# Kernel optimization log

Measured on AMD Instinct MI355X. Metric: run time of the kernel, lower is better.

Reference implementation:

```python
import math
import jax, jax.numpy as jnp
import numpy as np

HEADS = 8


def setup_inputs() -> dict:
    key = jax.random.key(0)
    ks = jax.random.split(key, 8)
    B, L, S, C = 2, 1024, 2048, 1280
    CORR = 256  # native seg_corr resolution; nearest-upsampled x4 to (1024, 1024)
    sc = 0.02
    return {
        "hidden_states": jax.random.normal(ks[0], (B, L, C), jnp.float32),
        "encoder_hidden_states": jax.random.normal(ks[1], (B, S, C), jnp.float32),
        "seg_corr": jax.random.randint(ks[2], (B, CORR, CORR), 0, 2, jnp.int32),
        "Wq": jax.random.normal(ks[3], (C, C), jnp.float32) * sc,
        "Wk": jax.random.normal(ks[4], (C, C), jnp.float32) * sc,
        "Wv": jax.random.normal(ks[5], (C, C), jnp.float32) * sc,
        "Wo": jax.random.normal(ks[6], (C, C), jnp.float32) * sc,
        "bo": jnp.zeros((C,), jnp.float32),
    }


def reference(hidden_states, encoder_hidden_states, seg_corr, Wq, Wk, Wv, Wo, bo):
    B, L, C = hidden_states.shape
    S = encoder_hidden_states.shape[1]
    H = HEADS
    d = C // H

    # projections -> [B, H, L, d] / [B, H, S, d]
    q = (hidden_states @ Wq).reshape(B, L, H, d).transpose(0, 2, 1, 3)
    k = (encoder_hidden_states @ Wk).reshape(B, S, H, d).transpose(0, 2, 1, 3)
    v = (encoder_hidden_states @ Wv).reshape(B, S, H, d).transpose(0, 2, 1, 3)

    scale = 1.0 / math.sqrt(d)
    scores = jnp.einsum("bhld,bhsd->bhls", q, k) * scale  # [B, H, L, S]

    half = S // 2  # S == 2L in the match-attention branch
    # nearest-neighbor upsample of seg_corr to (L, half) == integer repeat
    rL = L // seg_corr.shape[1]
    rS = half // seg_corr.shape[2]
    corr = jnp.repeat(jnp.repeat(seg_corr, rL, axis=1), rS, axis=2)[:, None]  # [B,1,L,half]

    # hard correlation mask on the second half of keys (reference-image tokens)
    masked = jnp.where(corr == 1, scores[..., half:], jnp.float32(-jnp.inf))
    scores = jnp.concatenate([scores[..., :half], masked], axis=-1)

    attn_weight = jax.nn.softmax(scores, axis=-1)  # dropout_p = 0.0
    out = jnp.einsum("bhls,bhsd->bhld", attn_weight, v)
    out = out.transpose(0, 2, 1, 3).reshape(B, L, C)

    out = out @ Wo + bo            # to_out[0]; to_out[1] dropout is identity at p=0
    out = out + hidden_states      # residual connection; rescale_output_factor = 1
    return out
```

## Files before the change

### kernel.cpp

```cpp
#include <hip/hip_runtime.h>

typedef unsigned short u16;
typedef unsigned int   u32;
typedef unsigned char  u8;

using bf16x8 = __attribute__((ext_vector_type(8))) __bf16;
using f32x4  = __attribute__((ext_vector_type(4))) float;

__device__ __forceinline__ u16 f2bf(float f) {
    u32 u = __float_as_uint(f);
    return (u16)((u + 0x7FFFu + ((u >> 16) & 1u)) >> 16);
}

#define MFMA(a, b, c) __builtin_amdgcn_mfma_f32_16x16x32_bf16((a), (b), (c), 0, 0, 0)
#define EXP2(x) __builtin_amdgcn_exp2f(x)

__device__ __forceinline__ void gll16(const u16* g, u16* l) {
    __builtin_amdgcn_global_load_lds(
        (const __attribute__((address_space(1))) void*)g,
        (__attribute__((address_space(3))) void*)l, 16, 0, 0);
}

__global__ __launch_bounds__(256) void wtrans_kernel(
    const float* __restrict__ W0, const float* __restrict__ W1,
    const float* __restrict__ W2, const float* __restrict__ W3,
    u16* __restrict__ T0, u16* __restrict__ T1,
    u16* __restrict__ T2, u16* __restrict__ T3) {
    const int N = 1280;
    const int z = blockIdx.z;
    const float* W = (z == 0) ? W0 : (z == 1) ? W1 : (z == 2) ? W2 : W3;
    u16* T = (z == 0) ? T0 : (z == 1) ? T1 : (z == 2) ? T2 : T3;
    __shared__ float t[32][33];
    const int bx = blockIdx.x * 32, by = blockIdx.y * 32;
    const int x = threadIdx.x, ty = threadIdx.y;
#pragma unroll
    for (int j = 0; j < 4; j++) {
        const int y = ty + j * 8;
        t[y][x] = W[(size_t)(by + y) * N + (bx + x)];
    }
    __syncthreads();
#pragma unroll
    for (int j = 0; j < 4; j++) {
        const int y = ty + j * 8;
        T[(size_t)(bx + y) * N + (by + x)] = f2bf(t[x][y]);
    }
}

__global__ __launch_bounds__(256) void conv2_kernel(const float* __restrict__ in0,
                                                    u16* __restrict__ out0,
                                                    const float* __restrict__ in1,
                                                    u16* __restrict__ out1) {
    const int bid = blockIdx.x;
    const float* in = (bid < 1280) ? in0 : in1;
    u16* out = (bid < 1280) ? out0 : out1;
    const int i = ((bid < 1280) ? bid : bid - 1280) * 256 + threadIdx.x;
    const float4 a = ((const float4*)in)[i * 2];
    const float4 b = ((const float4*)in)[i * 2 + 1];
    union { uint4 u; u16 s[8]; } cv;
    cv.s[0] = f2bf(a.x); cv.s[1] = f2bf(a.y); cv.s[2] = f2bf(a.z); cv.s[3] = f2bf(a.w);
    cv.s[4] = f2bf(b.x); cv.s[5] = f2bf(b.y); cv.s[6] = f2bf(b.z); cv.s[7] = f2bf(b.w);
    ((uint4*)out)[i] = cv.u;
}

template <int MI, bool TRANSC, bool EPI>
__global__ __launch_bounds__(256) void gemm2_kernel(
    const u16* __restrict__ A, const u16* __restrict__ Bt, void* __restrict__ Cp,
    const float* __restrict__ bias, const float* __restrict__ resid,
    const int M, const int N, const int K) {
    __shared__ __align__(16) u16 Al[2][MI * 32 * 64];
    __shared__ __align__(16) u16 Bl[2][128 * 64];
    const int tid = threadIdx.x;
    const int lane = tid & 63, w = tid >> 6;
    const int wr = w >> 1, wc = w & 1;
    const int lr = lane & 15, lq = lane >> 4;
    const int m0 = blockIdx.y * (MI * 32), n0 = blockIdx.x * 128;

    const int f_r = tid >> 3;
    const int srcch = (tid & 7) ^ ((tid >> 3) & 7);
    const int ldst = (tid & 192) * 8;

    const f32x4 fzero = {0.f, 0.f, 0.f, 0.f};
    f32x4 acc[MI][4];
#pragma unroll
    for (int i = 0; i < MI; i++)
#pragma unroll
        for (int j = 0; j < 4; j++) acc[i][j] = fzero;

    const int nkt = K >> 6;

#define STAGE(buf, kt)                                                          \
    {                                                                           \
        const int k0s = (kt) << 6;                                              \
        _Pragma("unroll")                                                       \
        for (int i = 0; i < MI; i++) {                                          \
            const int r = i * 32 + f_r;                                         \
            gll16(&A[(size_t)(m0 + r) * K + k0s + srcch * 8],                   \
                  &Al[buf][i * 2048 + ldst]);                                   \
        }                                                                       \
        _Pragma("unroll")                                                       \
        for (int i = 0; i < 4; i++) {                                           \
            const int r = i * 32 + f_r;                                         \
            gll16(&Bt[(size_t)(n0 + r) * K + k0s + srcch * 8],                  \
                  &Bl[buf][i * 2048 + ldst]);                                   \
        }                                                                       \
    }

    STAGE(0, 0);
    asm volatile("s_waitcnt vmcnt(0)" ::: "memory");
    __syncthreads();
    int cur = 0;
    for (int kt = 0; kt < nkt; kt++) {
        if (kt + 1 < nkt) STAGE(cur ^ 1, kt + 1);
#pragma unroll
        for (int ks = 0; ks < 2; ks++) {
            bf16x8 af[MI], bfv[4];
#pragma unroll
            for (int mi = 0; mi < MI; mi++) {
                const int rowA = wr * (MI * 16) + mi * 16 + lr;
                af[mi] = *(const bf16x8*)&Al[cur][rowA * 64 +
                                                  (((ks * 4 + lq) ^ (rowA & 7)) << 3)];
            }
#pragma unroll
            for (int ni = 0; ni < 4; ni++) {
                const int rowB = wc * 64 + ni * 16 + lr;
                bfv[ni] = *(const bf16x8*)&Bl[cur][rowB * 64 +
                                                   (((ks * 4 + lq) ^ (rowB & 7)) << 3)];
            }
#pragma unroll
            for (int mi = 0; mi < MI; mi++)
#pragma unroll
                for (int ni = 0; ni < 4; ni++)
                    acc[mi][ni] = MFMA(af[mi], bfv[ni], acc[mi][ni]);
        }
        asm volatile("s_waitcnt vmcnt(0)" ::: "memory");
        __syncthreads();
        cur ^= 1;
    }
#undef STAGE

#pragma unroll
    for (int mi = 0; mi < MI; mi++)
#pragma unroll
        for (int ni = 0; ni < 4; ni++)
#pragma unroll
            for (int j = 0; j < 4; j++) {
                const int row = m0 + wr * (MI * 16) + mi * 16 + lq * 4 + j;
                const int col = n0 + wc * 64 + ni * 16 + lr;
                const float v = acc[mi][ni][j];
                if (EPI) {
                    ((float*)Cp)[(size_t)row * N + col] =
                        v + bias[col] + resid[(size_t)row * N + col];
                } else if (TRANSC) {
                    ((u16*)Cp)[((size_t)(col >> 11) * 1280 + row) * 2048 +
                               (col & 2047)] = f2bf(v);
                } else {
                    ((u16*)Cp)[(size_t)row * N + col] = f2bf(v);
                }
            }
}

__global__ __launch_bounds__(256) void attn_kernel(
    const u16* __restrict__ qb, const u16* __restrict__ kb,
    const u16* __restrict__ vtb, const int* __restrict__ seg,
    u16* __restrict__ ao) {
    __shared__ __align__(16) u16 arena[14080];
    const int KL = 0;
    const int VT = 5376;
    const int PT = 11776;
    const int SG = 13056;
    u8* segl8 = (u8*)&arena[SG];

    const int tid = threadIdx.x;
    const int lane = tid & 63, w = tid >> 6;
    const int qg = w >> 1, kc = w & 1;
    const int lr = lane & 15, lq = lane >> 4;
    const int id = blockIdx.x;
    const int h = id & 7, bz = (id >> 3) & 1, qt = id >> 4;

#pragma unroll
    for (int i = 0; i < 2; i++) {
        const int4 v =
            *(const int4*)&seg[(size_t)(bz * 256 + qt * 8) * 256 + tid * 8 + i * 4];
        segl8[tid * 8 + i * 4 + 0] = (u8)v.x;
        segl8[tid * 8 + i * 4 + 1] = (u8)v.y;
        segl8[tid * 8 + i * 4 + 2] = (u8)v.z;
        segl8[tid * 8 + i * 4 + 3] = (u8)v.w;
    }

    bf16x8 qf[5];
    {
        const size_t qrow =
            (size_t)(bz * 1024 + qt * 32 + qg * 16 + lr) * 1280 + h * 160;
#pragma unroll
        for (int ks = 0; ks < 5; ks++)
            qf[ks] = *(const bf16x8*)&qb[qrow + ks * 32 + lq * 8];
    }

    const int nk0 = tid, nk1 = tid + 256;
    const int nv0 = tid, nv1 = tid + 256;
    const bool exK = (tid < 128);
    const int ne = exK ? (512 + tid) : (384 + tid);
    const int gok0 = (nk0 / 20) * 1280 + (nk0 % 20) * 8;
    const int lok0 = (nk0 / 20) * 168 + (nk0 % 20) * 8;
    const int gok1 = (nk1 / 20) * 1280 + (nk1 % 20) * 8;
    const int lok1 = (nk1 / 20) * 168 + (nk1 % 20) * 8;
    const int gov0 = (nv0 >> 2) * 2048 + (nv0 & 3) * 8;
    const int lov0 = (nv0 >> 2) * 40 + (nv0 & 3) * 8;
    const int gov1 = (nv1 >> 2) * 2048 + (nv1 & 3) * 8;
    const int lov1 = (nv1 >> 2) * 40 + (nv1 & 3) * 8;
    const int goe = exK ? ((ne / 20) * 1280 + (ne % 20) * 8)
                        : ((ne >> 2) * 2048 + (ne & 3) * 8);
    const int loe = exK ? ((ne / 20) * 168 + (ne % 20) * 8)
                        : ((ne >> 2) * 40 + (ne & 3) * 8);

    const u16* kP = kb + (size_t)(bz * 2048) * 1280 + h * 160;
    const u16* vP = vtb + (size_t)(bz * 1280 + h * 160) * 2048;

    const f32x4 fzero = {0.f, 0.f, 0.f, 0.f};
    f32x4 oacc[5];
#pragma unroll
    for (int d = 0; d < 5; d++) oacc[d] = fzero;
    f32x4 oaccL = fzero;
    const float sc2 = 0.11405508f;
    bf16x8 ones8;
#pragma unroll
    for (int e = 0; e < 8; e++) {
        const u16 one = 0x3F80;
        ones8[e] = *(const __bf16*)&one;
    }
    u16* ptq = &arena[PT + qg * 640];

    uint4 rk0 = *(const uint4*)&kP[gok0];
    uint4 rk1 = *(const uint4*)&kP[gok1];
    uint4 rv0 = *(const uint4*)&vP[gov0];
    uint4 rv1 = *(const uint4*)&vP[gov1];
    uint4 re  = exK ? *(const uint4*)&kP[goe] : *(const uint4*)&vP[goe];

    for (int kt = 0; kt < 64; kt++) {
        __syncthreads();
        *(uint4*)&arena[KL + lok0] = rk0;
        *(uint4*)&arena[KL + lok1] = rk1;
        *(uint4*)&arena[VT + lov0] = rv0;
        *(uint4*)&arena[VT + lov1] = rv1;
        if (exK) *(uint4*)&arena[KL + loe] = re;
        else     *(uint4*)&arena[VT + loe] = re;
        kP += 40960;
        vP += 32;
        __syncthreads();

        if (kt + 1 < 64) {
            rk0 = *(const uint4*)&kP[gok0];
            rk1 = *(const uint4*)&kP[gok1];
            rv0 = *(const uint4*)&vP[gov0];
            rv1 = *(const uint4*)&vP[gov1];
            re  = exK ? *(const uint4*)&kP[goe] : *(const uint4*)&vP[goe];
        }

        const u16* kbase = &arena[KL + (kc * 16 + lr) * 168 + lq * 8];
        f32x4 sA = fzero, sB = fzero;
        sA = MFMA(qf[0], *(const bf16x8*)&kbase[0],   sA);
        sB = MFMA(qf[1], *(const bf16x8*)&kbase[32],  sB);
        sA = MFMA(qf[2], *(const bf16x8*)&kbase[64],  sA);
        sB = MFMA(qf[3], *(const bf16x8*)&kbase[96],  sB);
        sA = MFMA(qf[4], *(const bf16x8*)&kbase[128], sA);

        float msk = 0.f;
        if (kt >= 32) {
            const int sg = (kt - 32) * 8 + kc * 4 + (lr >> 2);
            msk = segl8[(qg * 4 + lq) * 256 + sg] ? 0.f : -1e30f;
        }
#pragma unroll
        for (int j = 0; j < 4; j++) {
            const float e = EXP2(fmaf(sA[j] + sB[j], sc2, msk));
            *(__bf16*)&ptq[(lq * 4 + j) * 40 + kc * 16 + lr] = (__bf16)e;
        }
        __syncthreads();

        const bf16x8 pa = *(const bf16x8*)&ptq[lr * 40 + lq * 8];
        oaccL = MFMA(pa, ones8, oaccL);
#pragma unroll
        for (int nt2 = 0; nt2 < 5; nt2++) {
            const bf16x8 bv = *(const bf16x8*)
                &arena[VT + (kc * 80 + nt2 * 16 + lr) * 40 + lq * 8];
            oacc[nt2] = MFMA(pa, bv, oacc[nt2]);
        }
    }

    float inv[4];
#pragma unroll
    for (int j = 0; j < 4; j++) inv[j] = 1.f / oaccL[j];
#pragma unroll
    for (int nt2 = 0; nt2 < 5; nt2++)
#pragma unroll
        for (int j = 0; j < 4; j++) {
            const int row = qt * 32 + qg * 16 + lq * 4 + j;
            const int col = h * 160 + kc * 80 + nt2 * 16 + lr;
            *(__bf16*)&ao[(size_t)(bz * 1024 + row) * 1280 + col] =
                (__bf16)(oacc[nt2][j] * inv[j]);
        }
}

extern "C" void kernel_launch(void* const* d_in, const int* in_sizes, int n_in,
                              void* d_out, int out_size, void* d_ws, size_t ws_size,
                              hipStream_t stream) {
    const float* hs  = (const float*)d_in[0];
    const float* ehs = (const float*)d_in[1];
    const int*   seg = (const int*)d_in[2];
    const float* Wq  = (const float*)d_in[3];
    const float* Wk  = (const float*)d_in[4];
    const float* Wv  = (const float*)d_in[5];
    const float* Wo  = (const float*)d_in[6];
    const float* bo  = (const float*)d_in[7];
    float* out = (float*)d_out;

    u16* base  = (u16*)d_ws;
    u16* WoT   = base;
    u16* qbuf  = WoT + 1638400;
    u16* kbuf  = qbuf + 2621440;
    u16* vtbuf = kbuf + 5242880;
    u16* hbuf  = vtbuf + 5242880;
    u16* ebuf  = hbuf + 2621440;
    u16* WqT   = ebuf + 5242880;
    u16* WkT   = WqT + 1638400;
    u16* WvT   = WkT + 1638400;
    u16* aobuf = hbuf;

    dim3 tb(32, 8), tg(40, 40, 4);
    wtrans_kernel<<<tg, tb, 0, stream>>>(Wq, Wk, Wv, Wo, WqT, WkT, WvT, WoT);
    conv2_kernel<<<3840, 256, 0, stream>>>(hs, hbuf, ehs, ebuf);

    gemm2_kernel<1, false, false><<<dim3(10, 64), 256, 0, stream>>>(
        hbuf, WqT, qbuf, nullptr, nullptr, 2048, 1280, 1280);
    gemm2_kernel<2, false, false><<<dim3(10, 64), 256, 0, stream>>>(
        ebuf, WkT, kbuf, nullptr, nullptr, 4096, 1280, 1280);
    gemm2_kernel<2, true, false><<<dim3(32, 20), 256, 0, stream>>>(
        WvT, ebuf, vtbuf, nullptr, nullptr, 1280, 4096, 1280);

    attn_kernel<<<512, 256, 0, stream>>>(qbuf, kbuf, vtbuf, seg, aobuf);

    gemm2_kernel<1, false, true><<<dim3(10, 64), 256, 0, stream>>>(
        aobuf, WoT, out, bo, hs, 2048, 1280, 1280);
}
```

Baseline: 163.1 us.

## Double-buffer K/V tiles in LDS and make score tiles wave-private

The attention loop now keeps two LDS buffers for K and V^T and stores the next tile into the alternate buffer after the PV MFMAs. This cuts the loop to one block barrier per iteration instead of three. Each wave now computes both 16-key halves of the score tile itself, with a per-wave P scratch area, so the barrier between softmax and the PV MFMA is no longer needed. The cost is that QK work is duplicated across the two kc waves of each query group, and LDS use roughly doubles, which may lower occupancy.

```diff
diff --git a/kernel.cpp b/kernel.cpp
--- a/kernel.cpp
+++ b/kernel.cpp
@@ -163,11 +163,10 @@
     const u16* __restrict__ qb, const u16* __restrict__ kb,
     const u16* __restrict__ vtb, const int* __restrict__ seg,
     u16* __restrict__ ao) {
-    __shared__ __align__(16) u16 arena[14080];
-    const int KL = 0;
+    __shared__ __align__(16) u16 arena[27136];
     const int VT = 5376;
-    const int PT = 11776;
-    const int SG = 13056;
+    const int PT = 23552;
+    const int SG = 26112;
     u8* segl8 = (u8*)&arena[SG];
 
     const int tid = threadIdx.x;
@@ -205,13 +204,13 @@
     const int gok1 = (nk1 / 20) * 1280 + (nk1 % 20) * 8;
     const int lok1 = (nk1 / 20) * 168 + (nk1 % 20) * 8;
     const int gov0 = (nv0 >> 2) * 2048 + (nv0 & 3) * 8;
-    const int lov0 = (nv0 >> 2) * 40 + (nv0 & 3) * 8;
+    const int lov0 = VT + (nv0 >> 2) * 40 + (nv0 & 3) * 8;
     const int gov1 = (nv1 >> 2) * 2048 + (nv1 & 3) * 8;
-    const int lov1 = (nv1 >> 2) * 40 + (nv1 & 3) * 8;
+    const int lov1 = VT + (nv1 >> 2) * 40 + (nv1 & 3) * 8;
     const int goe = exK ? ((ne / 20) * 1280 + (ne % 20) * 8)
                         : ((ne >> 2) * 2048 + (ne & 3) * 8);
     const int loe = exK ? ((ne / 20) * 168 + (ne % 20) * 8)
-                        : ((ne >> 2) * 40 + (ne & 3) * 8);
+                        : (VT + (ne >> 2) * 40 + (ne & 3) * 8);
 
     const u16* kP = kb + (size_t)(bz * 2048) * 1280 + h * 160;
     const u16* vP = vtb + (size_t)(bz * 1280 + h * 160) * 2048;
@@ -228,62 +227,77 @@
         const u16 one = 0x3F80;
         ones8[e] = *(const __bf16*)&one;
     }
-    u16* ptq = &arena[PT + qg * 640];
+    u16* ptw = &arena[PT + w * 640];
 
     uint4 rk0 = *(const uint4*)&kP[gok0];
     uint4 rk1 = *(const uint4*)&kP[gok1];
     uint4 rv0 = *(const uint4*)&vP[gov0];
     uint4 rv1 = *(const uint4*)&vP[gov1];
     uint4 re  = exK ? *(const uint4*)&kP[goe] : *(const uint4*)&vP[goe];
-
+    *(uint4*)&arena[lok0] = rk0;
+    *(uint4*)&arena[lok1] = rk1;
+    *(uint4*)&arena[lov0] = rv0;
+    *(uint4*)&arena[lov1] = rv1;
+    if (exK) *(uint4*)&arena[loe] = re;
+    else     *(uint4*)&arena[loe] = re;
+    kP += 40960;
+    vP += 32;
+    __syncthreads();
+
+    int cb = 0;
     for (int kt = 0; kt < 64; kt++) {
-        __syncthreads();
-        *(uint4*)&arena[KL + lok0] = rk0;
-        *(uint4*)&arena[KL + lok1] = rk1;
-        *(uint4*)&arena[VT + lov0] = rv0;
-        *(uint4*)&arena[VT + lov1] = rv1;
-        if (exK) *(uint4*)&arena[KL + loe] = re;
-        else     *(uint4*)&arena[VT + loe] = re;
-        kP += 40960;
-        vP += 32;
-        __syncthreads();
-
         if (kt + 1 < 64) {
             rk0 = *(const uint4*)&kP[gok0];
             rk1 = *(const uint4*)&kP[gok1];
             rv0 = *(const uint4*)&vP[gov0];
             rv1 = *(const uint4*)&vP[gov1];
             re  = exK ? *(const uint4*)&kP[goe] : *(const uint4*)&vP[goe];
-        }
-
-        const u16* kbase = &arena[KL + (kc * 16 + lr) * 168 + lq * 8];
-        f32x4 sA = fzero, sB = fzero;
-        sA = MFMA(qf[0], *(const bf16x8*)&kbase[0],   sA);
-        sB = MFMA(qf[1], *(const bf16x8*)&kbase[32],  sB);
-        sA = MFMA(qf[2], *(const bf16x8*)&kbase[64],  sA);
-        sB = MFMA(qf[3], *(const bf16x8*)&kbase[96],  sB);
-        sA = MFMA(qf[4], *(const bf16x8*)&kbase[128], sA);
-
-        float msk = 0.f;
+            kP += 40960;
+            vP += 32;
+        }
+
+        const u16* kbase = &arena[cb + lr * 168 + lq * 8];
+        f32x4 s0 = fzero, s1 = fzero;
+#pragma unroll
+        for (int ks = 0; ks < 5; ks++) {
+            s0 = MFMA(qf[ks], *(const bf16x8*)&kbase[ks * 32], s0);
+            s1 = MFMA(qf[ks], *(const bf16x8*)&kbase[16 * 168 + ks * 32], s1);
+        }
+
+        float msk0 = 0.f, msk1 = 0.f;
         if (kt >= 32) {
-            const int sg = (kt - 32) * 8 + kc * 4 + (lr >> 2);
-            msk = segl8[(qg * 4 + lq) * 256 + sg] ? 0.f : -1e30f;
+            const int sgb = (kt - 32) * 8 + (lr >> 2);
+            const int qrow4 = (qg * 4 + lq) * 256;
+            msk0 = segl8[qrow4 + sgb] ? 0.f : -1e30f;
+            msk1 = segl8[qrow4 + sgb + 4] ? 0.f : -1e30f;
         }
 #pragma unroll
         for (int j = 0; j < 4; j++) {
-            const float e = EXP2(fmaf(sA[j] + sB[j], sc2, msk));
-            *(__bf16*)&ptq[(lq * 4 + j) * 40 + kc * 16 + lr] = (__bf16)e;
-        }
-        __syncthreads();
-
-        const bf16x8 pa = *(const bf16x8*)&ptq[lr * 40 + lq * 8];
+            const float p0 = EXP2(fmaf(s0[j], sc2, msk0));
+            const float p1 = EXP2(fmaf(s1[j], sc2, msk1));
+            *(__bf16*)&ptw[(lq * 4 + j) * 40 + lr] = (__bf16)p0;
+            *(__bf16*)&ptw[(lq * 4 + j) * 40 + 16 + lr] = (__bf16)p1;
+        }
+
+        const bf16x8 pa = *(const bf16x8*)&ptw[lr * 40 + lq * 8];
         oaccL = MFMA(pa, ones8, oaccL);
 #pragma unroll
         for (int nt2 = 0; nt2 < 5; nt2++) {
             const bf16x8 bv = *(const bf16x8*)
-                &arena[VT + (kc * 80 + nt2 * 16 + lr) * 40 + lq * 8];
+                &arena[cb + VT + (kc * 80 + nt2 * 16 + lr) * 40 + lq * 8];
             oacc[nt2] = MFMA(pa, bv, oacc[nt2]);
         }
+
+        if (kt + 1 < 64) {
+            const int nb = cb ^ 11776;
+            *(uint4*)&arena[nb + lok0] = rk0;
+            *(uint4*)&arena[nb + lok1] = rk1;
+            *(uint4*)&arena[nb + lov0] = rv0;
+            *(uint4*)&arena[nb + lov1] = rv1;
+            *(uint4*)&arena[nb + loe] = re;
+        }
+        __syncthreads();
+        cb ^= 11776;
     }
 
     float inv[4];
```

New measurement: 169.7 us. 4.0% more time.
